# Performance work log

Hardware: AMD Instinct MI355X
Metric: run time of the kernel (lower is better)

Reference implementation:

```python
import jax, jax.numpy as jnp
import numpy as np
import math

DIM = 1024
NUM_HEADS = 16
HEAD_DIM = DIM // NUM_HEADS
EPS = 1e-6
DILATED = 2
WINDOW = 2  # window_size init arg; actual window = L * WINDOW per side


def setup_inputs() -> dict:
    key = jax.random.key(0)
    ks = jax.random.split(key, 14)
    B, S = 1, 8704
    x = jax.random.normal(ks[0], (B, S, DIM), jnp.float32)
    ang = jax.random.uniform(ks[1], (S, HEAD_DIM // 2), jnp.float32, -jnp.pi, jnp.pi)
    freqs_cos = jnp.cos(ang)
    freqs_sin = jnp.sin(ang)
    def lin(k):
        return 0.02 * jax.random.normal(k, (DIM, DIM), jnp.float32)
    def bias(k):
        return 0.01 * jax.random.normal(k, (DIM,), jnp.float32)
    return {
        'x': x, 'freqs_cos': freqs_cos, 'freqs_sin': freqs_sin,
        'wq': lin(ks[2]), 'bq': bias(ks[3]),
        'wk': lin(ks[4]), 'bk': bias(ks[5]),
        'wv': lin(ks[6]), 'bv': bias(ks[7]),
        'wo': lin(ks[8]), 'bo': bias(ks[9]),
        'gq': 1.0 + 0.02 * jax.random.normal(ks[10], (DIM,), jnp.float32),
        'gk': 1.0 + 0.02 * jax.random.normal(ks[11], (DIM,), jnp.float32),
        'f': 34, 'L': 256,
    }


def rmsnorm(h, g):
    return h * jax.lax.rsqrt(jnp.mean(h * h, axis=-1, keepdims=True) + EPS) * g


def rope(h, cos, sin):
    # h: [B,S,D] viewed as interleaved complex pairs per head, rotated by unit freqs
    B, S, D = h.shape
    hp = h.reshape(B, S, NUM_HEADS, HEAD_DIM // 2, 2)
    a, b = hp[..., 0], hp[..., 1]
    c = cos[None, :, None, :]
    s = sin[None, :, None, :]
    ra = a * c - b * s
    rb = a * s + b * c
    return jnp.stack([ra, rb], axis=-1).reshape(B, S, D)


def windowed_attention(q, k, v, w):
    # sliding-window attention: query i attends keys j with |i-j| <= w (inclusive)
    B, S, D = q.shape
    H, hd = NUM_HEADS, HEAD_DIM
    def heads(t):
        return t.reshape(B, S, H, hd).transpose(0, 2, 1, 3)  # [B,H,S,hd]
    qh, kh, vh = heads(q), heads(k), heads(v)
    C = w  # block size == window -> only 3 neighbor key blocks per query block
    pad = (-S) % C
    Sp = S + pad
    nb = Sp // C
    def blocks(t):
        return jnp.pad(t, ((0, 0), (0, 0), (0, pad), (0, 0))).reshape(B, H, nb, C, hd)
    qb = blocks(qh)
    def win(t):
        tb = jnp.pad(blocks(t), ((0, 0), (0, 0), (1, 1), (0, 0), (0, 0)))
        return jnp.concatenate([tb[:, :, i:i + nb] for i in range(3)], axis=3)  # [B,H,nb,3C,hd]
    kw_, vw_ = win(kh), win(vh)
    scores = jnp.einsum('bhnqd,bhnkd->bhnqk', qb, kw_) * (1.0 / math.sqrt(hd))
    qi = jnp.arange(nb)[:, None, None] * C + jnp.arange(C)[None, :, None]      # [nb,C,1]
    kj = (jnp.arange(nb)[:, None, None] - 1) * C + jnp.arange(3 * C)[None, None, :]  # [nb,1,3C]
    valid = (kj >= 0) & (kj < S) & (qi - kj <= w) & (kj - qi <= w)
    scores = jnp.where(valid, scores, -1e9)
    p = jax.nn.softmax(scores, axis=-1)
    o = jnp.einsum('bhnqk,bhnkd->bhnqd', p, vw_)
    return o.reshape(B, H, Sp, hd)[:, :, :S].transpose(0, 2, 1, 3).reshape(B, S, D)


def reference(x, freqs_cos, freqs_sin, wq, bq, wk, bk, wv, bv, wo, bo, gq, gk, f, L):
    B, S, D = x.shape
    q = rope(rmsnorm(x @ wq + bq, gq), freqs_cos, freqs_sin)
    k = rope(rmsnorm(x @ wk + bk, gk), freqs_cos, freqs_sin)
    v = x @ wv + bv
    w = L * WINDOW
    use_dilated = DILATED > 1 and S // (DILATED * L) > 1
    if use_dilated:
        blk = DILATED * L
        pad_len = blk - S % blk  # == blk when S % blk == 0 (faithful to torch code)
        Sp = S + pad_len
        n = Sp // blk
        def padd(t):
            return jnp.pad(t, ((0, 0), (0, pad_len), (0, 0)))
        def dil(t):
            # 'b (n d l) c -> (b d) (n l) c'
            return t.reshape(B, n, DILATED, L, D).transpose(0, 2, 1, 3, 4).reshape(B * DILATED, n * L, D)
        q, k, v = dil(padd(q)), dil(padd(k)), dil(padd(v))
    o = windowed_attention(q, k, v, w)
    out = o @ wo + bo
    if use_dilated:
        # '(b d) (n l) c -> b (n d l) c', then drop pad
        out = out.reshape(B, DILATED, n, L, D).transpose(0, 2, 1, 3, 4).reshape(B, n * DILATED * L, D)
        out = out[:, :S]
    return out
```

## Files before the change

kernel.cpp:

```cpp
#include <hip/hip_runtime.h>
#include <hip/hip_bf16.h>
#include <stdint.h>

#define DIM 1024
#define NH 16
#define HD 64
#define S_ORIG 8704
#define WIN 512

typedef __attribute__((ext_vector_type(8))) short short8;
typedef __attribute__((ext_vector_type(4))) float f32x4;

__device__ __forceinline__ float bf2f(unsigned short u) {
    return __uint_as_float(((unsigned int)u) << 16);
}
__device__ __forceinline__ unsigned short f2bf(float f) {
    unsigned int x = __float_as_uint(f);
    unsigned int r = x + 0x7fffu + ((x >> 16) & 1u);
    return (unsigned short)(r >> 16);
}
__device__ __forceinline__ unsigned int cvtpk(float lo, float hi) {
    unsigned int r;
    asm("v_cvt_pk_bf16_f32 %0, %1, %2" : "=v"(r) : "v"(lo), "v"(hi));
    return r;
}
__device__ __forceinline__ float fexp2(float x) {
#if __has_builtin(__builtin_amdgcn_exp2f)
    return __builtin_amdgcn_exp2f(x);
#else
    float r;
    asm("v_exp_f32 %0, %1" : "=v"(r) : "v"(x));
    return r;
#endif
}

#define GLD_LDS(gptr, lptr) \
    __builtin_amdgcn_global_load_lds((const __attribute__((address_space(1))) void*)(gptr), \
                                     (__attribute__((address_space(3))) void*)(lptr), 16, 0, 0)

__global__ __launch_bounds__(256) void prep(const float* __restrict__ x,
                                            unsigned short* __restrict__ xb,
                                            const float* __restrict__ w0,
                                            const float* __restrict__ w1,
                                            const float* __restrict__ w2,
                                            const float* __restrict__ w3,
                                            unsigned short* __restrict__ wt) {
    __shared__ float ts[64][65];
    const int bx = blockIdx.x;
    const int t = threadIdx.x;
    if (bx < 8704) {
        int i = (bx * 256 + t) * 4;
        float4 v = *(const float4*)(x + i);
        ushort4 o;
        o.x = f2bf(v.x); o.y = f2bf(v.y); o.z = f2bf(v.z); o.w = f2bf(v.w);
        *(ushort4*)(xb + i) = o;
        return;
    }
    const int b = bx - 8704;
    const int z = b >> 8;
    const int rem = b & 255;
    const int kb = (rem >> 4) * 64, nb = (rem & 15) * 64;
    const float* w = z == 0 ? w0 : z == 1 ? w1 : z == 2 ? w2 : w3;
    unsigned short* o = wt + (size_t)z * DIM * DIM;
    const int c = t & 63, r4 = t >> 6;
#pragma unroll
    for (int rr = 0; rr < 16; rr++) {
        int row = rr * 4 + r4;
        ts[row][c] = w[(size_t)(kb + row) * DIM + nb + c];
    }
    __syncthreads();
#pragma unroll
    for (int rr = 0; rr < 16; rr++) {
        int nl = rr * 4 + r4;
        o[(size_t)(nb + nl) * DIM + kb + c] = f2bf(ts[c][nl]);
    }
}

template <int OUTF32>
__global__ __launch_bounds__(256) void gemm_bf16(const unsigned short* __restrict__ A,
                                                 const unsigned short* __restrict__ Bt,
                                                 const float* __restrict__ b0,
                                                 const float* __restrict__ b1,
                                                 const float* __restrict__ b2,
                                                 void* __restrict__ Cout) {
    __shared__ __align__(16) unsigned short As[128 * 32];
    __shared__ __align__(16) unsigned short Bs[128 * 32];
    const int z = blockIdx.z;
    const unsigned short* B = Bt + (size_t)z * DIM * DIM;
    const float* bias = z == 0 ? b0 : (z == 1 ? b1 : b2);
    const int m0 = blockIdx.x * 128, n0 = blockIdx.y * 128;
    const int tid = threadIdx.x;
    const int lane = tid & 63, wv = tid >> 6;
    const int wr = wv >> 1, wc = wv & 1;
    const int quad = lane >> 4, r = lane & 15;

    f32x4 acc[4][4];
#pragma unroll
    for (int i = 0; i < 4; i++)
#pragma unroll
        for (int j = 0; j < 4; j++)
#pragma unroll
            for (int t4 = 0; t4 < 4; t4++) acc[i][j][t4] = 0.0f;

    const unsigned short* a_base = A + (size_t)m0 * DIM;
    const unsigned short* b_base = B + (size_t)n0 * DIM;
    const int c0 = wv * 128 + lane;
    const int r0 = c0 >> 2, o0 = (((c0 & 3) ^ ((c0 >> 3) & 3))) * 8;
    const int c1 = c0 + 64;
    const int r1 = c1 >> 2, o1 = (((c1 & 3) ^ ((c1 >> 3) & 3))) * 8;
    unsigned short* lA0 = &As[(size_t)(wv * 128) * 8];
    unsigned short* lA1 = &As[(size_t)(wv * 128 + 64) * 8];
    unsigned short* lB0 = &Bs[(size_t)(wv * 128) * 8];
    unsigned short* lB1 = &Bs[(size_t)(wv * 128 + 64) * 8];

    const int jsw = (quad ^ ((r >> 1) & 3)) * 8;

    for (int k0 = 0; k0 < DIM; k0 += 32) {
        __syncthreads();
        GLD_LDS(a_base + (size_t)r0 * DIM + k0 + o0, lA0);
        GLD_LDS(a_base + (size_t)r1 * DIM + k0 + o1, lA1);
        GLD_LDS(b_base + (size_t)r0 * DIM + k0 + o0, lB0);
        GLD_LDS(b_base + (size_t)r1 * DIM + k0 + o1, lB1);
        __syncthreads();
        short8 af[4], bfr[4];
#pragma unroll
        for (int i = 0; i < 4; i++)
            af[i] = *(const short8*)&As[(wr * 64 + i * 16 + r) * 32 + jsw];
#pragma unroll
        for (int j = 0; j < 4; j++)
            bfr[j] = *(const short8*)&Bs[(wc * 64 + j * 16 + r) * 32 + jsw];
#pragma unroll
        for (int i = 0; i < 4; i++)
#pragma unroll
            for (int j = 0; j < 4; j++)
                acc[i][j] = __builtin_amdgcn_mfma_f32_16x16x32_bf16(af[i], bfr[j], acc[i][j], 0, 0, 0);
    }

#pragma unroll
    for (int i = 0; i < 4; i++) {
        const int row = m0 + wr * 64 + i * 16 + quad * 4;
#pragma unroll
        for (int j = 0; j < 4; j++) {
            const int col = n0 + wc * 64 + j * 16 + r;
            const float bvl = bias[col];
#pragma unroll
            for (int t4 = 0; t4 < 4; t4++) {
                float vv = acc[i][j][t4] + bvl;
                if (OUTF32) {
                    ((float*)Cout)[(size_t)(row + t4) * DIM + col] = vv;
                } else {
                    ((unsigned short*)Cout)[(size_t)z * S_ORIG * DIM + (size_t)(row + t4) * DIM + col] = f2bf(vv);
                }
            }
        }
    }
}

__global__ __launch_bounds__(256) void norm_rope(unsigned short* __restrict__ hq,
                                                 unsigned short* __restrict__ hk,
                                                 const float* __restrict__ gq,
                                                 const float* __restrict__ gk,
                                                 const float* __restrict__ fcos,
                                                 const float* __restrict__ fsin) {
    const int z = blockIdx.y;
    unsigned short* h = z == 0 ? hq : hk;
    const float* g = z == 0 ? gq : gk;
    const int w = threadIdx.x >> 6, lane = threadIdx.x & 63;
    const int srow = blockIdx.x * 4 + w;
    unsigned short* hp = h + (size_t)srow * DIM;
    const int p0 = lane * 8, p1 = 512 + lane * 8;

    union { int4 i4; unsigned short u[8]; } r0, r1, o0, o1;
    r0.i4 = *(const int4*)(hp + p0);
    r1.i4 = *(const int4*)(hp + p1);
    float v[16];
#pragma unroll
    for (int j = 0; j < 8; j++) { v[j] = bf2f(r0.u[j]); v[8 + j] = bf2f(r1.u[j]); }

    float ss = 0.0f;
#pragma unroll
    for (int j = 0; j < 16; j++) ss += v[j] * v[j];
#pragma unroll
    for (int off = 1; off < 64; off <<= 1) ss += __shfl_xor(ss, off, 64);
    const float rinv = rsqrtf(ss * (1.0f / DIM) + 1e-6f);

    float4 ga = *(const float4*)(g + p0), gb = *(const float4*)(g + p0 + 4);
    float4 gc = *(const float4*)(g + p1), gd = *(const float4*)(g + p1 + 4);
    const float* gg[4] = {&ga.x, &gb.x, &gc.x, &gd.x};
#pragma unroll
    for (int q4 = 0; q4 < 4; q4++)
#pragma unroll
        for (int j = 0; j < 4; j++) v[q4 * 4 + j] *= rinv * gg[q4][j];

    const int i0 = (p0 & 63) >> 1;
    float4 cs = *(const float4*)(fcos + (size_t)srow * 32 + i0);
    float4 sn = *(const float4*)(fsin + (size_t)srow * 32 + i0);
    const float* cp = &cs.x;
    const float* sp = &sn.x;
#pragma unroll
    for (int seg = 0; seg < 2; seg++) {
        unsigned short* uo = seg == 0 ? o0.u : o1.u;
#pragma unroll
        for (int pr = 0; pr < 4; pr++) {
            const float a = v[seg * 8 + pr * 2], b = v[seg * 8 + pr * 2 + 1];
            uo[pr * 2]     = f2bf(a * cp[pr] - b * sp[pr]);
            uo[pr * 2 + 1] = f2bf(a * sp[pr] + b * cp[pr]);
        }
    }
    *(int4*)(hp + p0) = o0.i4;
    *(int4*)(hp + p1) = o1.i4;
}

__global__ __launch_bounds__(256) void attn(const unsigned short* __restrict__ qkv,
                                            unsigned short* __restrict__ ob) {
    __shared__ __align__(16) unsigned short Ks[64 * 72];
    __shared__ __align__(16) unsigned short Vt[64 * 72];
    __shared__ __align__(16) unsigned short Ps[4][16 * 72];

    const int head = blockIdx.x >> 1;
    const int d = blockIdx.x & 1;
    const int qt = blockIdx.y;
    const int tid = threadIdx.x;
    const int lane = tid & 63, wv = tid >> 6;
    const int quad = lane >> 4, r16 = lane & 15;

    const unsigned short* qb = qkv;
    const unsigned short* kb = qkv + (size_t)S_ORIG * DIM;
    const unsigned short* vb = qkv + (size_t)2 * S_ORIG * DIM;

    const int qi = qt * 64 + wv * 16 + r16;
    const int og_q = ((qi >> 8) << 9) + d * 256 + (qi & 255);
    short8 qf[2];
    {
        const float QSC = 0.125f * 1.44269504088896f;
        const unsigned short* qrow = qb + (size_t)og_q * DIM + head * HD + quad * 8;
#pragma unroll
        for (int c = 0; c < 2; c++) {
            union { int4 i4; unsigned short u[8]; short8 s8; } in, outv;
            in.i4 = *(const int4*)(qrow + c * 32);
#pragma unroll
            for (int j = 0; j < 8; j++) outv.u[j] = f2bf(bf2f(in.u[j]) * QSC);
            qf[c] = outv.s8;
        }
    }

    f32x4 oacc[4];
    float lsum = 0.0f;
#pragma unroll
    for (int nt = 0; nt < 4; nt++)
#pragma unroll
        for (int rr = 0; rr < 4; rr++) oacc[nt][rr] = 0.0f;

    const int kt_lo = (qt - 8 > 0) ? (qt - 8) : 0;
    const int kt_hi = (qt + 8 < 67) ? (qt + 8) : 67;

    const int st_row0 = tid >> 3, st_ch = (tid & 7) * 8;
    const int vt_kk = (tid & 31) * 2, vt_d0 = (tid >> 5) * 8;

    for (int kt = kt_lo; kt <= kt_hi; kt++) {
        const int kbase = kt * 64;
        __syncthreads();

#pragma unroll
        for (int half = 0; half < 2; half++) {
            const int row = st_row0 + half * 32;
            const int kj = kbase + row;
            const int ok = ((kj >> 8) << 9) + d * 256 + (kj & 255);
            *(int4*)&Ks[row * 72 + st_ch] = *(const int4*)(kb + (size_t)ok * DIM + head * HD + st_ch);
        }
        {
            const int kj0 = kbase + vt_kk;
            const int ok0 = ((kj0 >> 8) << 9) + d * 256 + (kj0 & 255);
            union { int4 i4; unsigned int w[4]; } a0, a1;
            a0.i4 = *(const int4*)(vb + (size_t)ok0 * DIM + head * HD + vt_d0);
            a1.i4 = *(const int4*)(vb + (size_t)(ok0 + 1) * DIM + head * HD + vt_d0);
#pragma unroll
            for (int dw = 0; dw < 4; dw++) {
                unsigned int lo = __builtin_amdgcn_perm(a1.w[dw], a0.w[dw], 0x05040100u);
                unsigned int hi = __builtin_amdgcn_perm(a1.w[dw], a0.w[dw], 0x07060302u);
                *(unsigned int*)&Vt[(vt_d0 + dw * 2) * 72 + vt_kk] = lo;
                *(unsigned int*)&Vt[(vt_d0 + dw * 2 + 1) * 72 + vt_kk] = hi;
            }
        }
        __syncthreads();

        f32x4 sv[4];
#pragma unroll
        for (int nt = 0; nt < 4; nt++) {
            short8 k0f = *(const short8*)&Ks[(nt * 16 + r16) * 72 + quad * 8];
            short8 k1f = *(const short8*)&Ks[(nt * 16 + r16) * 72 + 32 + quad * 8];
            f32x4 a = {0.0f, 0.0f, 0.0f, 0.0f};
            a = __builtin_amdgcn_mfma_f32_16x16x32_bf16(k0f, qf[0], a, 0, 0, 0);
            a = __builtin_amdgcn_mfma_f32_16x16x32_bf16(k1f, qf[1], a, 0, 0, 0);
            sv[nt] = a;
        }

        const bool edge = (kt == qt - 8) || (kt == qt + 8);
        unsigned short* pw = &Ps[wv][0];
#pragma unroll
        for (int nt = 0; nt < 4; nt++) {
            float p[4];
#pragma unroll
            for (int rr = 0; rr < 4; rr++) {
                float e = fexp2(sv[nt][rr]);
                if (edge) {
                    const int kj = kbase + nt * 16 + quad * 4 + rr;
                    const int dl = qi - kj;
                    if (dl > WIN || dl < -WIN) e = 0.0f;
                }
                p[rr] = e;
            }
            lsum += (p[0] + p[1]) + (p[2] + p[3]);
            uint2 pk;
            pk.x = cvtpk(p[0], p[1]);
            pk.y = cvtpk(p[2], p[3]);
            *(uint2*)&pw[r16 * 72 + nt * 16 + quad * 4] = pk;
        }
        __asm__ volatile("s_waitcnt lgkmcnt(0)" ::: "memory");

        short8 pf0 = *(const short8*)&pw[r16 * 72 + quad * 8];
        short8 pf1 = *(const short8*)&pw[r16 * 72 + 32 + quad * 8];
#pragma unroll
        for (int nt = 0; nt < 4; nt++) {
            short8 v0f = *(const short8*)&Vt[(nt * 16 + r16) * 72 + quad * 8];
            short8 v1f = *(const short8*)&Vt[(nt * 16 + r16) * 72 + 32 + quad * 8];
            oacc[nt] = __builtin_amdgcn_mfma_f32_16x16x32_bf16(v0f, pf0, oacc[nt], 0, 0, 0);
            oacc[nt] = __builtin_amdgcn_mfma_f32_16x16x32_bf16(v1f, pf1, oacc[nt], 0, 0, 0);
        }
    }

    lsum += __shfl_xor(lsum, 16, 64);
    lsum += __shfl_xor(lsum, 32, 64);
    {
        const int cnt = (qi + WIN < 4607 ? qi + WIN : 4607) - 4351;
        if (cnt > 0) lsum += (float)cnt;
    }
    const float linv = 1.0f / lsum;

#pragma unroll
    for (int nt = 0; nt < 4; nt++) {
        ushort4 o;
        o.x = f2bf(oacc[nt][0] * linv);
        o.y = f2bf(oacc[nt][1] * linv);
        o.z = f2bf(oacc[nt][2] * linv);
        o.w = f2bf(oacc[nt][3] * linv);
        *(ushort4*)&ob[(size_t)og_q * DIM + head * HD + nt * 16 + quad * 4] = o;
    }
}

extern "C" void kernel_launch(void* const* d_in, const int* in_sizes, int n_in,
                              void* d_out, int out_size, void* d_ws, size_t ws_size,
                              hipStream_t stream) {
    const float* x    = (const float*)d_in[0];
    const float* fcos = (const float*)d_in[1];
    const float* fsin = (const float*)d_in[2];
    const float* wq   = (const float*)d_in[3];
    const float* bq   = (const float*)d_in[4];
    const float* wk   = (const float*)d_in[5];
    const float* bk   = (const float*)d_in[6];
    const float* wv   = (const float*)d_in[7];
    const float* bv   = (const float*)d_in[8];
    const float* wo   = (const float*)d_in[9];
    const float* bo   = (const float*)d_in[10];
    const float* gq   = (const float*)d_in[11];
    const float* gk   = (const float*)d_in[12];

    char* ws = (char*)d_ws;
    unsigned short* xb = (unsigned short*)(ws);
    unsigned short* wt = (unsigned short*)(ws + 17825792);
    unsigned short* h  = (unsigned short*)(ws + 26214400);
    unsigned short* ob = (unsigned short*)(ws + 79691776);
    float* outp = (float*)d_out;

    prep<<<9728, 256, 0, stream>>>(x, xb, wq, wk, wv, wo, wt);
    gemm_bf16<0><<<dim3(68, 8, 3), 256, 0, stream>>>(xb, wt, bq, bk, bv, (void*)h);
    norm_rope<<<dim3(2176, 2), 256, 0, stream>>>(h, h + (size_t)S_ORIG * DIM, gq, gk, fcos, fsin);
    attn<<<dim3(32, 68), 256, 0, stream>>>(h, ob);
    gemm_bf16<1><<<dim3(68, 8, 1), 256, 0, stream>>>(ob, wt + (size_t)3 * DIM * DIM, bo, bo, bo, (void*)outp);
}
```

Baseline: 321.5 us.

## Process two query tiles per attention block and load K via swizzled direct-to-LDS

Each attention workgroup now handles two adjacent 64-row query tiles, so every K/V tile staged in shared memory is reused by both tiles and the grid is halved. This cuts global K/V traffic and the number of staging barriers per query. K is loaded with a direct global-to-LDS path into an unpadded, XOR-swizzled layout instead of a padded one. The cost is more registers per thread for the second accumulator set, and half as many workgroups to fill the GPU.

```diff
diff --git a/kernel.cpp b/kernel.cpp
--- a/kernel.cpp
+++ b/kernel.cpp
@@ -211,15 +211,64 @@
     *(int4*)(hp + p1) = o1.i4;
 }
 
+__device__ __forceinline__ void qstep(const unsigned short* __restrict__ Ks,
+                                      const unsigned short* __restrict__ Vt,
+                                      unsigned short* __restrict__ pw,
+                                      int jsw0, int jsw1, int quad, int r16,
+                                      int kbase, int qi, bool edge,
+                                      const short8* __restrict__ qf,
+                                      f32x4* __restrict__ oacc, float& lsum) {
+    f32x4 sv[4];
+#pragma unroll
+    for (int nt = 0; nt < 4; nt++) {
+        const int row = (nt * 16 + r16) * 64;
+        short8 k0f = *(const short8*)&Ks[row + jsw0];
+        short8 k1f = *(const short8*)&Ks[row + jsw1];
+        f32x4 a = {0.0f, 0.0f, 0.0f, 0.0f};
+        a = __builtin_amdgcn_mfma_f32_16x16x32_bf16(k0f, qf[0], a, 0, 0, 0);
+        a = __builtin_amdgcn_mfma_f32_16x16x32_bf16(k1f, qf[1], a, 0, 0, 0);
+        sv[nt] = a;
+    }
+#pragma unroll
+    for (int nt = 0; nt < 4; nt++) {
+        float p[4];
+#pragma unroll
+        for (int rr = 0; rr < 4; rr++) {
+            float e = fexp2(sv[nt][rr]);
+            if (edge) {
+                const int kj = kbase + nt * 16 + quad * 4 + rr;
+                const int dl = qi - kj;
+                if (dl > WIN || dl < -WIN) e = 0.0f;
+            }
+            p[rr] = e;
+        }
+        lsum += (p[0] + p[1]) + (p[2] + p[3]);
+        uint2 pk;
+        pk.x = cvtpk(p[0], p[1]);
+        pk.y = cvtpk(p[2], p[3]);
+        *(uint2*)&pw[r16 * 72 + nt * 16 + quad * 4] = pk;
+    }
+    __asm__ volatile("s_waitcnt lgkmcnt(0)" ::: "memory");
+    short8 pf0 = *(const short8*)&pw[r16 * 72 + quad * 8];
+    short8 pf1 = *(const short8*)&pw[r16 * 72 + 32 + quad * 8];
+#pragma unroll
+    for (int nt = 0; nt < 4; nt++) {
+        short8 v0f = *(const short8*)&Vt[(nt * 16 + r16) * 72 + quad * 8];
+        short8 v1f = *(const short8*)&Vt[(nt * 16 + r16) * 72 + 32 + quad * 8];
+        oacc[nt] = __builtin_amdgcn_mfma_f32_16x16x32_bf16(v0f, pf0, oacc[nt], 0, 0, 0);
+        oacc[nt] = __builtin_amdgcn_mfma_f32_16x16x32_bf16(v1f, pf1, oacc[nt], 0, 0, 0);
+    }
+}
+
 __global__ __launch_bounds__(256) void attn(const unsigned short* __restrict__ qkv,
                                             unsigned short* __restrict__ ob) {
-    __shared__ __align__(16) unsigned short Ks[64 * 72];
+    __shared__ __align__(16) unsigned short Ks[64 * 64];
     __shared__ __align__(16) unsigned short Vt[64 * 72];
     __shared__ __align__(16) unsigned short Ps[4][16 * 72];
 
     const int head = blockIdx.x >> 1;
     const int d = blockIdx.x & 1;
-    const int qt = blockIdx.y;
+    const int t0 = blockIdx.y * 2, t1 = t0 + 1;
     const int tid = threadIdx.x;
     const int lane = tid & 63, wv = tid >> 6;
     const int quad = lane >> 4, r16 = lane & 15;
@@ -228,45 +277,63 @@
     const unsigned short* kb = qkv + (size_t)S_ORIG * DIM;
     const unsigned short* vb = qkv + (size_t)2 * S_ORIG * DIM;
 
-    const int qi = qt * 64 + wv * 16 + r16;
-    const int og_q = ((qi >> 8) << 9) + d * 256 + (qi & 255);
-    short8 qf[2];
+    const int qi0 = t0 * 64 + wv * 16 + r16;
+    const int qi1 = qi0 + 64;
+    const int og_q0 = ((qi0 >> 8) << 9) + d * 256 + (qi0 & 255);
+    const int og_q1 = ((qi1 >> 8) << 9) + d * 256 + (qi1 & 255);
+    short8 qf0[2], qf1[2];
     {
         const float QSC = 0.125f * 1.44269504088896f;
-        const unsigned short* qrow = qb + (size_t)og_q * DIM + head * HD + quad * 8;
+        const unsigned short* qr0 = qb + (size_t)og_q0 * DIM + head * HD + quad * 8;
+        const unsigned short* qr1 = qb + (size_t)og_q1 * DIM + head * HD + quad * 8;
 #pragma unroll
         for (int c = 0; c < 2; c++) {
-            union { int4 i4; unsigned short u[8]; short8 s8; } in, outv;
-            in.i4 = *(const int4*)(qrow + c * 32);
-#pragma unroll
-            for (int j = 0; j < 8; j++) outv.u[j] = f2bf(bf2f(in.u[j]) * QSC);
-            qf[c] = outv.s8;
-        }
-    }
-
-    f32x4 oacc[4];
-    float lsum = 0.0f;
+            union { int4 i4; unsigned short u[8]; short8 s8; } i0v, i1v, a0v, a1v;
+            i0v.i4 = *(const int4*)(qr0 + c * 32);
+            i1v.i4 = *(const int4*)(qr1 + c * 32);
+#pragma unroll
+            for (int j = 0; j < 8; j++) {
+                a0v.u[j] = f2bf(bf2f(i0v.u[j]) * QSC);
+                a1v.u[j] = f2bf(bf2f(i1v.u[j]) * QSC);
+            }
+            qf0[c] = a0v.s8;
+            qf1[c] = a1v.s8;
+        }
+    }
+
+    f32x4 oacc0[4], oacc1[4];
+    float lsum0 = 0.0f, lsum1 = 0.0f;
 #pragma unroll
     for (int nt = 0; nt < 4; nt++)
 #pragma unroll
-        for (int rr = 0; rr < 4; rr++) oacc[nt][rr] = 0.0f;
-
-    const int kt_lo = (qt - 8 > 0) ? (qt - 8) : 0;
-    const int kt_hi = (qt + 8 < 67) ? (qt + 8) : 67;
-
-    const int st_row0 = tid >> 3, st_ch = (tid & 7) * 8;
+        for (int rr = 0; rr < 4; rr++) { oacc0[nt][rr] = 0.0f; oacc1[nt][rr] = 0.0f; }
+
+    const int kt_lo = (t0 - 8 > 0) ? (t0 - 8) : 0;
+    const int kt_hi = (t1 + 8 < 67) ? (t1 + 8) : 67;
+
+    const int krow0 = tid >> 3;
+    const int kgc = ((tid & 7) ^ (krow0 & 7)) * 8;
+    unsigned short* kdst0 = &Ks[(size_t)(wv * 64) * 8];
+    unsigned short* kdst1 = &Ks[(size_t)(256 + wv * 64) * 8];
+
     const int vt_kk = (tid & 31) * 2, vt_d0 = (tid >> 5) * 8;
+
+    const int jsw0 = (quad ^ (r16 & 7)) * 8;
+    const int jsw1 = jsw0 ^ 32;
+
+    unsigned short* pw = &Ps[wv][0];
 
     for (int kt = kt_lo; kt <= kt_hi; kt++) {
         const int kbase = kt * 64;
         __syncthreads();
 
-#pragma unroll
-        for (int half = 0; half < 2; half++) {
-            const int row = st_row0 + half * 32;
-            const int kj = kbase + row;
-            const int ok = ((kj >> 8) << 9) + d * 256 + (kj & 255);
-            *(int4*)&Ks[row * 72 + st_ch] = *(const int4*)(kb + (size_t)ok * DIM + head * HD + st_ch);
+        {
+            const int kj0 = kbase + krow0;
+            const int ok0 = ((kj0 >> 8) << 9) + d * 256 + (kj0 & 255);
+            GLD_LDS(kb + (size_t)ok0 * DIM + head * HD + kgc, kdst0);
+            const int kj1 = kj0 + 32;
+            const int ok1 = ((kj1 >> 8) << 9) + d * 256 + (kj1 & 255);
+            GLD_LDS(kb + (size_t)ok1 * DIM + head * HD + kgc, kdst1);
         }
         {
             const int kj0 = kbase + vt_kk;
@@ -284,67 +351,40 @@
         }
         __syncthreads();
 
-        f32x4 sv[4];
-#pragma unroll
-        for (int nt = 0; nt < 4; nt++) {
-            short8 k0f = *(const short8*)&Ks[(nt * 16 + r16) * 72 + quad * 8];
-            short8 k1f = *(const short8*)&Ks[(nt * 16 + r16) * 72 + 32 + quad * 8];
-            f32x4 a = {0.0f, 0.0f, 0.0f, 0.0f};
-            a = __builtin_amdgcn_mfma_f32_16x16x32_bf16(k0f, qf[0], a, 0, 0, 0);
-            a = __builtin_amdgcn_mfma_f32_16x16x32_bf16(k1f, qf[1], a, 0, 0, 0);
-            sv[nt] = a;
-        }
-
-        const bool edge = (kt == qt - 8) || (kt == qt + 8);
-        unsigned short* pw = &Ps[wv][0];
-#pragma unroll
-        for (int nt = 0; nt < 4; nt++) {
-            float p[4];
-#pragma unroll
-            for (int rr = 0; rr < 4; rr++) {
-                float e = fexp2(sv[nt][rr]);
-                if (edge) {
-                    const int kj = kbase + nt * 16 + quad * 4 + rr;
-                    const int dl = qi - kj;
-                    if (dl > WIN || dl < -WIN) e = 0.0f;
-                }
-                p[rr] = e;
-            }
-            lsum += (p[0] + p[1]) + (p[2] + p[3]);
-            uint2 pk;
-            pk.x = cvtpk(p[0], p[1]);
-            pk.y = cvtpk(p[2], p[3]);
-            *(uint2*)&pw[r16 * 72 + nt * 16 + quad * 4] = pk;
-        }
-        __asm__ volatile("s_waitcnt lgkmcnt(0)" ::: "memory");
-
-        short8 pf0 = *(const short8*)&pw[r16 * 72 + quad * 8];
-        short8 pf1 = *(const short8*)&pw[r16 * 72 + 32 + quad * 8];
-#pragma unroll
-        for (int nt = 0; nt < 4; nt++) {
-            short8 v0f = *(const short8*)&Vt[(nt * 16 + r16) * 72 + quad * 8];
-            short8 v1f = *(const short8*)&Vt[(nt * 16 + r16) * 72 + 32 + quad * 8];
-            oacc[nt] = __builtin_amdgcn_mfma_f32_16x16x32_bf16(v0f, pf0, oacc[nt], 0, 0, 0);
-            oacc[nt] = __builtin_amdgcn_mfma_f32_16x16x32_bf16(v1f, pf1, oacc[nt], 0, 0, 0);
-        }
-    }
-
-    lsum += __shfl_xor(lsum, 16, 64);
-    lsum += __shfl_xor(lsum, 32, 64);
+        if (kt <= t0 + 8)
+            qstep(Ks, Vt, pw, jsw0, jsw1, quad, r16, kbase, qi0,
+                  (kt == t0 - 8) || (kt == t0 + 8), qf0, oacc0, lsum0);
+        if (kt >= t1 - 8)
+            qstep(Ks, Vt, pw, jsw0, jsw1, quad, r16, kbase, qi1,
+                  (kt == t1 - 8) || (kt == t1 + 8), qf1, oacc1, lsum1);
+    }
+
+    lsum0 += __shfl_xor(lsum0, 16, 64);
+    lsum0 += __shfl_xor(lsum0, 32, 64);
+    lsum1 += __shfl_xor(lsum1, 16, 64);
+    lsum1 += __shfl_xor(lsum1, 32, 64);
     {
-        const int cnt = (qi + WIN < 4607 ? qi + WIN : 4607) - 4351;
-        if (cnt > 0) lsum += (float)cnt;
-    }
-    const float linv = 1.0f / lsum;
+        const int cnt0 = (qi0 + WIN < 4607 ? qi0 + WIN : 4607) - 4351;
+        if (cnt0 > 0) lsum0 += (float)cnt0;
+        const int cnt1 = (qi1 + WIN < 4607 ? qi1 + WIN : 4607) - 4351;
+        if (cnt1 > 0) lsum1 += (float)cnt1;
+    }
+    const float linv0 = 1.0f / lsum0;
+    const float linv1 = 1.0f / lsum1;
 
 #pragma unroll
     for (int nt = 0; nt < 4; nt++) {
-        ushort4 o;
-        o.x = f2bf(oacc[nt][0] * linv);
-        o.y = f2bf(oacc[nt][1] * linv);
-        o.z = f2bf(oacc[nt][2] * linv);
-        o.w = f2bf(oacc[nt][3] * linv);
-        *(ushort4*)&ob[(size_t)og_q * DIM + head * HD + nt * 16 + quad * 4] = o;
+        ushort4 o0, o1;
+        o0.x = f2bf(oacc0[nt][0] * linv0);
+        o0.y = f2bf(oacc0[nt][1] * linv0);
+        o0.z = f2bf(oacc0[nt][2] * linv0);
+        o0.w = f2bf(oacc0[nt][3] * linv0);
+        *(ushort4*)&ob[(size_t)og_q0 * DIM + head * HD + nt * 16 + quad * 4] = o0;
+        o1.x = f2bf(oacc1[nt][0] * linv1);
+        o1.y = f2bf(oacc1[nt][1] * linv1);
+        o1.z = f2bf(oacc1[nt][2] * linv1);
+        o1.w = f2bf(oacc1[nt][3] * linv1);
+        *(ushort4*)&ob[(size_t)og_q1 * DIM + head * HD + nt * 16 + quad * 4] = o1;
     }
 }
 
@@ -375,6 +415,6 @@
     prep<<<9728, 256, 0, stream>>>(x, xb, wq, wk, wv, wo, wt);
     gemm_bf16<0><<<dim3(68, 8, 3), 256, 0, stream>>>(xb, wt, bq, bk, bv, (void*)h);
     norm_rope<<<dim3(2176, 2), 256, 0, stream>>>(h, h + (size_t)S_ORIG * DIM, gq, gk, fcos, fsin);
-    attn<<<dim3(32, 68), 256, 0, stream>>>(h, ob);
+    attn<<<dim3(32, 34), 256, 0, stream>>>(h, ob);
     gemm_bf16<1><<<dim3(68, 8, 1), 256, 0, stream>>>(ob, wt + (size_t)3 * DIM * DIM, bo, bo, bo, (void*)outp);
 }
```

Measured after the change: 312.6 us. 2.8% less time.
